# Optimization experiments

Hardware: AMD Instinct MI355X
Metric: run time of the kernel (lower is better)

## Reference

```python
import jax, jax.numpy as jnp
import numpy as np

B, C, H, W_SP = 16, 128, 112, 112  # C doubles as nb_steps (time axis)
KH = 3
TAU_MEM = 1e-3
TAU_SYN = 1e-3
TIME_STEP = 1e-3
ALPHA = float(np.exp(-TIME_STEP / TAU_SYN))
BETA = float(np.exp(-TIME_STEP / TAU_MEM))


def setup_inputs() -> dict:
    key = jax.random.key(0)
    k1, k2 = jax.random.split(key)
    x = jax.random.normal(k1, (B, C, H, W_SP), dtype=jnp.float32)
    # kaiming_uniform_(a=0, mode='fan_in', nonlinearity='linear'): bound = sqrt(3) * 1/sqrt(fan_in)
    fan_in = C * KH * KH
    bound = float(np.sqrt(3.0 / fan_in))
    W = jax.random.uniform(k2, (C, C, KH, KH), minval=-bound, maxval=bound, dtype=jnp.float32)
    b = jnp.zeros((C,), dtype=jnp.float32)
    return {"x": x, "W": W, "b": b}


def reference(x, W, b):
    # Conv2d(in_channel, in_channel, kernel=3, stride=1, padding=1)
    y = jax.lax.conv_general_dilated(
        x, W, window_strides=(1, 1), padding=((1, 1), (1, 1)),
        dimension_numbers=("NCHW", "OIHW", "NCHW")) + b[None, :, None, None]
    conv_shape = y.shape
    Bsz, T = y.shape[0], y.shape[1]  # T == nb_steps (channel axis reused as time)
    X = y.reshape(Bsz, T, -1)  # (B, T, H*W)
    # FFT of leakage kernels: l = alpha^t, k = beta^t * (1 - beta)
    t = jnp.arange(T, dtype=jnp.float32)
    l = jnp.power(jnp.float32(ALPHA), t)
    k = jnp.power(jnp.float32(BETA), t) * (1.0 - jnp.float32(BETA))
    fft_l_k = jnp.fft.rfft(l, n=2 * T) * jnp.fft.rfft(k, n=2 * T)  # (T+1,)
    # Parallel leaky integration via linear (causal) convolution in frequency domain
    fft_X = jnp.fft.rfft(X, n=2 * T, axis=1)  # (B, T+1, H*W) complex
    mem = jnp.fft.irfft(fft_X * fft_l_k[None, :, None], n=2 * T, axis=1)[:, :T]
    return mem.reshape(conv_shape)
```

## Files before the change

kernel.cpp:

```cpp
#include <hip/hip_runtime.h>

typedef __attribute__((ext_vector_type(8))) short s16x8;
typedef __attribute__((ext_vector_type(4))) float f32x4;

#define ALPHA_F 0.36787944117144233f
#define BETA_F  0.36787944117144233f
#define OMB_F   0.63212055882855767f

__device__ __forceinline__ unsigned short f2bf(float f){
  union { float f; unsigned int u; } v; v.f = f;
  unsigned int u = v.u;
  return (unsigned short)((u + 0x7FFFu + ((u >> 16) & 1u)) >> 16);
}
__device__ __forceinline__ float bf2f(unsigned short s){
  union { unsigned int u; float f; } v; v.u = ((unsigned int)s) << 16;
  return v.f;
}

__global__ __launch_bounds__(256) void reorder_w(const float* __restrict__ W,
                                                 unsigned short* __restrict__ Wr){
  int f = blockIdx.x * 256 + threadIdx.x;
  if (f >= 9*128*128) return;
  int cil = f & 31;
  int co  = (f >> 5) & 127;
  int cic = (f >> 12) & 3;
  int pos = f >> 14;
  int ci  = (cic << 5) | cil;
  Wr[f] = f2bf(W[(co*128 + ci)*9 + pos]);
}

__global__ __launch_bounds__(256) void x_to_cl(const float* __restrict__ x,
                                               unsigned short* __restrict__ xcl){
  __shared__ unsigned short ls[128*113];
  int b = blockIdx.x / 112, h = blockIdx.x % 112;
  const float* xp = x + (size_t)b*1605632 + h*112;
  for (int u = threadIdx.x; u < 128*112; u += 256){
    int ci = u / 112, w = u - ci*112;
    ls[ci*113 + w] = f2bf(xp[ci*12544 + w]);
  }
  __syncthreads();
  unsigned short* op = xcl + (size_t)(b*112 + h) * (112*128);
  for (int u = threadIdx.x; u < 112*64; u += 256){
    int pix = u >> 6, cp = u & 63;
    ushort2 v;
    v.x = ls[(2*cp  )*113 + pix];
    v.y = ls[(2*cp+1)*113 + pix];
    *(ushort2*)(op + pix*128 + 2*cp) = v;
  }
}

__global__ __launch_bounds__(256, 2) void conv_lif(
    const unsigned short* __restrict__ xcl,
    const unsigned short* __restrict__ Wr,
    const float* __restrict__ bias,
    float* __restrict__ out)
{
  __shared__ unsigned short sm[128*132];
  const int tid  = threadIdx.x;
  const int lane = tid & 63;
  const int wid  = tid >> 6;
  const int wm   = wid & 1;
  const int wn   = wid >> 1;
  const int l15  = lane & 15;
  const int quad = lane >> 4;
  const int bz = blockIdx.z;
  const int h0 = blockIdx.y * 8, w0 = blockIdx.x * 16;

  f32x4 acc[4][4];
  #pragma unroll
  for (int i=0;i<4;i++)
    #pragma unroll
    for (int j=0;j<4;j++) acc[i][j] = (f32x4){0.f,0.f,0.f,0.f};

  const unsigned short* xb = xcl + (size_t)bz * (112*112*128);

  for (int cic = 0; cic < 4; ++cic){
    __syncthreads();
    const int ci0 = cic << 5;
    #pragma unroll
    for (int it = 0; it < 6; ++it){
      int u = tid + it*256;
      if (u < 1440){
        int posidx = u >> 3, cq = u & 7;
        int r = posidx / 18, c = posidx - r*18;
        int gh = h0 - 1 + r, gw = w0 - 1 + c;
        ushort4 val = make_ushort4(0,0,0,0);
        if (gh >= 0 && gh < 112 && gw >= 0 && gw < 112)
          val = *(const ushort4*)(xb + ((gh*112 + gw) << 7) + ci0 + (cq << 2));
        *(ushort4*)(sm + posidx*32 + (cq << 2)) = val;
      }
    }
    __syncthreads();
    #pragma unroll
    for (int pos = 0; pos < 9; ++pos){
      const int dh = pos/3, dw = pos - dh*3;
      const unsigned short* wb = Wr + (((pos<<2) + cic) << 12) + (wm<<11)
                                    + (l15<<5) + (quad<<3);
      s16x8 af[4];
      #pragma unroll
      for (int mt=0; mt<4; ++mt)
        af[mt] = *(const s16x8*)(wb + (mt<<9));
      #pragma unroll
      for (int nt=0; nt<4; ++nt){
        int rr = (wn<<2) + nt;
        const unsigned short* bp = sm + ((rr+dh)*18 + (l15+dw))*32 + (quad<<3);
        s16x8 bfr = *(const s16x8*)bp;
        #pragma unroll
        for (int mt=0; mt<4; ++mt)
          acc[mt][nt] = __builtin_amdgcn_mfma_f32_16x16x32_bf16(af[mt], bfr, acc[mt][nt], 0, 0, 0);
      }
    }
  }

  __syncthreads();
  #pragma unroll
  for (int mt=0; mt<4; ++mt){
    int cobase = (wm<<6) + (mt<<4) + (quad<<2);
    float4 bv = *(const float4*)(bias + cobase);
    #pragma unroll
    for (int nt=0; nt<4; ++nt){
      int pix = (((wn<<2)+nt)<<4) + l15;
      f32x4 a = acc[mt][nt];
      ushort4 w4;
      w4.x = f2bf(a.x + bv.x);
      w4.y = f2bf(a.y + bv.y);
      w4.z = f2bf(a.z + bv.z);
      w4.w = f2bf(a.w + bv.w);
      *(ushort4*)(sm + pix*132 + cobase) = w4;
    }
  }
  __syncthreads();

  if (tid < 128){
    int r = tid >> 4, c = tid & 15;
    float s = 0.f, m = 0.f;
    float* op = out + (size_t)bz*1605632 + (h0 + r)*112 + (w0 + c);
    const unsigned short* yr = sm + tid*132;
    #pragma unroll 8
    for (int t = 0; t < 128; ++t){
      float y = bf2f(yr[t]);
      s = ALPHA_F * s + y;
      m = BETA_F  * m + OMB_F * s;
      op[(size_t)t*12544] = m;
    }
  }
}

extern "C" void kernel_launch(void* const* d_in, const int* in_sizes, int n_in,
                              void* d_out, int out_size, void* d_ws, size_t ws_size,
                              hipStream_t stream){
  const float* x = (const float*)d_in[0];
  const float* W = (const float*)d_in[1];
  const float* b = (const float*)d_in[2];
  float* out = (float*)d_out;
  unsigned short* Wr  = (unsigned short*)d_ws;
  unsigned short* xcl = (unsigned short*)((char*)d_ws + (1 << 20));
  reorder_w<<<576, 256, 0, stream>>>(W, Wr);
  x_to_cl<<<16*112, 256, 0, stream>>>(x, xcl);
  conv_lif<<<dim3(7, 14, 16), 256, 0, stream>>>(xcl, Wr, b, out);
}
```

Measured before the change: 288.0 us.

## Pad LDS strides, vectorize transpose, raise occupancy, split LIF scan across threads

The transpose kernel now reads x with float4 loads and writes channel-last bf16 output as 8-element vectors through a padded LDS tile. The conv kernel pads its LDS strides (36 for the input tile, 130 for the output tile) to cut bank conflicts, and raises launch_bounds min-blocks from 2 to 3 since the smaller LDS footprint allows it. The LIF scan now uses all 256 threads: the second half starts 16 steps early as warm-up, which works because alpha and beta are about 0.37 and the state decays quickly. That warm-up is an approximation with a small truncation error, and the third block per CU may force register spills.

```diff
diff --git a/kernel.cpp b/kernel.cpp
--- a/kernel.cpp
+++ b/kernel.cpp
@@ -1,11 +1,15 @@
 #include <hip/hip_runtime.h>
 
 typedef __attribute__((ext_vector_type(8))) short s16x8;
+typedef __attribute__((ext_vector_type(8))) unsigned short u16x8;
 typedef __attribute__((ext_vector_type(4))) float f32x4;
 
 #define ALPHA_F 0.36787944117144233f
 #define BETA_F  0.36787944117144233f
 #define OMB_F   0.63212055882855767f
+
+#define XS_STRIDE 36
+#define YS_STRIDE 130
 
 __device__ __forceinline__ unsigned short f2bf(float f){
   union { float f; unsigned int u; } v; v.f = f;
@@ -31,31 +35,43 @@
 
 __global__ __launch_bounds__(256) void x_to_cl(const float* __restrict__ x,
                                                unsigned short* __restrict__ xcl){
-  __shared__ unsigned short ls[128*113];
-  int b = blockIdx.x / 112, h = blockIdx.x % 112;
+  __shared__ unsigned short ls[112*129];
+  const int tid = threadIdx.x;
+  const int b = blockIdx.x / 112, h = blockIdx.x % 112;
   const float* xp = x + (size_t)b*1605632 + h*112;
-  for (int u = threadIdx.x; u < 128*112; u += 256){
-    int ci = u / 112, w = u - ci*112;
-    ls[ci*113 + w] = f2bf(xp[ci*12544 + w]);
+  const int q = tid & 31;
+  const int cih = tid >> 5;
+  if (q < 28){
+    #pragma unroll
+    for (int p = 0; p < 16; ++p){
+      int ci = (p << 3) + cih;
+      float4 v = *(const float4*)(xp + ci*12544 + (q << 2));
+      int w0 = q << 2;
+      ls[(w0  )*129 + ci] = f2bf(v.x);
+      ls[(w0+1)*129 + ci] = f2bf(v.y);
+      ls[(w0+2)*129 + ci] = f2bf(v.z);
+      ls[(w0+3)*129 + ci] = f2bf(v.w);
+    }
   }
   __syncthreads();
   unsigned short* op = xcl + (size_t)(b*112 + h) * (112*128);
-  for (int u = threadIdx.x; u < 112*64; u += 256){
-    int pix = u >> 6, cp = u & 63;
-    ushort2 v;
-    v.x = ls[(2*cp  )*113 + pix];
-    v.y = ls[(2*cp+1)*113 + pix];
-    *(ushort2*)(op + pix*128 + 2*cp) = v;
+  for (int u = tid; u < 112*16; u += 256){
+    int pix = u >> 4, cp = u & 15;
+    const unsigned short* lr = ls + pix*129 + (cp << 3);
+    u16x8 v;
+    #pragma unroll
+    for (int j = 0; j < 8; ++j) v[j] = lr[j];
+    *(u16x8*)(op + (pix << 7) + (cp << 3)) = v;
   }
 }
 
-__global__ __launch_bounds__(256, 2) void conv_lif(
+__global__ __launch_bounds__(256, 3) void conv_lif(
     const unsigned short* __restrict__ xcl,
     const unsigned short* __restrict__ Wr,
     const float* __restrict__ bias,
     float* __restrict__ out)
 {
-  __shared__ unsigned short sm[128*132];
+  __shared__ unsigned short sm[128*YS_STRIDE];
   const int tid  = threadIdx.x;
   const int lane = tid & 63;
   const int wid  = tid >> 6;
@@ -87,7 +103,7 @@
         ushort4 val = make_ushort4(0,0,0,0);
         if (gh >= 0 && gh < 112 && gw >= 0 && gw < 112)
           val = *(const ushort4*)(xb + ((gh*112 + gw) << 7) + ci0 + (cq << 2));
-        *(ushort4*)(sm + posidx*32 + (cq << 2)) = val;
+        *(ushort4*)(sm + posidx*XS_STRIDE + (cq << 2)) = val;
       }
     }
     __syncthreads();
@@ -103,7 +119,7 @@
       #pragma unroll
       for (int nt=0; nt<4; ++nt){
         int rr = (wn<<2) + nt;
-        const unsigned short* bp = sm + ((rr+dh)*18 + (l15+dw))*32 + (quad<<3);
+        const unsigned short* bp = sm + ((rr+dh)*18 + (l15+dw))*XS_STRIDE + (quad<<3);
         s16x8 bfr = *(const s16x8*)bp;
         #pragma unroll
         for (int mt=0; mt<4; ++mt)
@@ -121,27 +137,33 @@
     for (int nt=0; nt<4; ++nt){
       int pix = (((wn<<2)+nt)<<4) + l15;
       f32x4 a = acc[mt][nt];
-      ushort4 w4;
-      w4.x = f2bf(a.x + bv.x);
-      w4.y = f2bf(a.y + bv.y);
-      w4.z = f2bf(a.z + bv.z);
-      w4.w = f2bf(a.w + bv.w);
-      *(ushort4*)(sm + pix*132 + cobase) = w4;
+      ushort2 w01, w23;
+      w01.x = f2bf(a.x + bv.x);
+      w01.y = f2bf(a.y + bv.y);
+      w23.x = f2bf(a.z + bv.z);
+      w23.y = f2bf(a.w + bv.w);
+      unsigned short* yp = sm + pix*YS_STRIDE + cobase;
+      *(ushort2*)(yp)     = w01;
+      *(ushort2*)(yp + 2) = w23;
     }
   }
   __syncthreads();
 
-  if (tid < 128){
-    int r = tid >> 4, c = tid & 15;
+  {
+    int pix  = tid & 127;
+    int half = tid >> 7;
+    int r = pix >> 4, c = pix & 15;
     float s = 0.f, m = 0.f;
     float* op = out + (size_t)bz*1605632 + (h0 + r)*112 + (w0 + c);
-    const unsigned short* yr = sm + tid*132;
-    #pragma unroll 8
-    for (int t = 0; t < 128; ++t){
+    const unsigned short* yr = sm + pix*YS_STRIDE;
+    int t0    = half ? 48 : 0;
+    int tstore= half ? 64 : 0;
+    int tend  = half ? 128 : 64;
+    for (int t = t0; t < tend; ++t){
       float y = bf2f(yr[t]);
       s = ALPHA_F * s + y;
       m = BETA_F  * m + OMB_F * s;
-      op[(size_t)t*12544] = m;
+      if (t >= tstore) op[(size_t)t*12544] = m;
     }
   }
 }
```

After: 297.8 us. +3.4%, slower.
